# Optimization experiments

Hardware: AMD Instinct MI355X
Metric: run time of the kernel (lower is better)

Reference implementation:

```python
import jax, jax.numpy as jnp
import numpy as np


def _sage_layer(x, src, dst, W_self, W_neigh, b, n_nodes):
    # mean aggregation over incoming edges: agg[v] = mean(x[u] for (u,v) in E)
    agg = jax.ops.segment_sum(x[src], dst, num_segments=n_nodes)          # [N, D]
    cnt = jax.ops.segment_sum(jnp.ones((src.shape[0],), x.dtype), dst,
                              num_segments=n_nodes)                        # [N]
    agg = agg / jnp.clip(cnt, 1.0)[:, None]
    # h = ReLU(x W_self^T + agg W_neigh^T + b)   (torch Linear weight is [out, in])
    h = jnp.einsum('nd,od->no', x, W_self) + jnp.einsum('nd,od->no', agg, W_neigh) + b
    return jax.nn.relu(h)


def setup_inputs() -> dict:
    key = jax.random.key(0)
    ks = jax.random.split(key, 7)
    N, E = 50000, 800000
    F_IN, H, F_OUT = 128, 256, 128
    x = jax.random.normal(ks[0], (N, F_IN), dtype=jnp.float32)
    edge_index = jax.random.randint(ks[1], (2, E), 0, N, dtype=jnp.int64)
    s = 0.05
    return {
        'x': x,
        'edge_index': edge_index,
        'W_self1': jax.random.normal(ks[2], (H, F_IN), dtype=jnp.float32) * s,
        'W_neigh1': jax.random.normal(ks[3], (H, F_IN), dtype=jnp.float32) * s,
        'b1': jnp.zeros((H,), dtype=jnp.float32),
        'W_self2': jax.random.normal(ks[4], (F_OUT, H), dtype=jnp.float32) * s,
        'W_neigh2': jax.random.normal(ks[5], (F_OUT, H), dtype=jnp.float32) * s,
        'b2': jnp.zeros((F_OUT,), dtype=jnp.float32),
    }


def reference(x, edge_index, W_self1, W_neigh1, b1, W_self2, W_neigh2, b2):
    n_nodes = x.shape[0]
    src, dst = edge_index[0], edge_index[1]
    h = _sage_layer(x, src, dst, W_self1, W_neigh1, b1, n_nodes)
    # dropout is identity at inference
    h = _sage_layer(h, src, dst, W_self2, W_neigh2, b2, n_nodes)
    return h
```

## Files before the change

kernel.cpp:

```cpp
#include <hip/hip_runtime.h>


#define CAP 64
#define CPAD 16

typedef __attribute__((ext_vector_type(8))) short bfrag;
typedef __attribute__((ext_vector_type(4))) float ffrag;

__device__ inline unsigned short f2bf(float f) {
    union { float f; unsigned u; } v; v.f = f;
    unsigned r = (v.u + 0x7FFFu + ((v.u >> 16) & 1u)) >> 16;
    return (unsigned short)r;
}

__global__ __launch_bounds__(256) void fill_direct(const int* __restrict__ src,
                                                   const int* __restrict__ dst,
                                                   int* __restrict__ cnt,
                                                   int* __restrict__ adj, int E) {
    int e = blockIdx.x * 256 + threadIdx.x;
    if (e >= E) return;
    int d = dst[e];
    int r = atomicAdd(&cnt[d * CPAD], 1);
    if (r < CAP) adj[d * CAP + r] = src[e];
}

__global__ __launch_bounds__(256) void cast_f32_bf16(const float* __restrict__ in,
                                                     unsigned short* __restrict__ outp,
                                                     long n4) {
    long i = (long)blockIdx.x * 256 + threadIdx.x;
    if (i >= n4) return;
    float4 v = *(const float4*)(in + i * 4);
    ushort4 o;
    o.x = f2bf(v.x); o.y = f2bf(v.y); o.z = f2bf(v.z); o.w = f2bf(v.w);
    *(ushort4*)(outp + i * 4) = o;
}

__global__ __launch_bounds__(256) void cast_weights(
        const float* __restrict__ W0, const float* __restrict__ W1,
        const float* __restrict__ W2, const float* __restrict__ W3,
        unsigned short* __restrict__ O0, unsigned short* __restrict__ O1,
        unsigned short* __restrict__ O2, unsigned short* __restrict__ O3) {
    int i = blockIdx.x * 256 + threadIdx.x;
    int sel = i >> 13, off = i & 8191;
    const float* src = (sel == 0) ? W0 : (sel == 1) ? W1 : (sel == 2) ? W2 : W3;
    unsigned short* dst = (sel == 0) ? O0 : (sel == 1) ? O1 : (sel == 2) ? O2 : O3;
    float4 v = ((const float4*)src)[off];
    ushort4 o;
    o.x = f2bf(v.x); o.y = f2bf(v.y); o.z = f2bf(v.z); o.w = f2bf(v.w);
    ((ushort4*)dst)[off] = o;
}

#define BFLO(u) __uint_as_float((u) << 16)
#define BFHI(u) __uint_as_float((u) & 0xFFFF0000u)

__global__ __launch_bounds__(256) void gather_mean_bf16(
        const unsigned short* __restrict__ Xb, const int* __restrict__ cnt,
        const int* __restrict__ adj, unsigned short* __restrict__ aggb, int N) {
    int gw = (blockIdx.x * 256 + threadIdx.x) >> 6;
    int lane = threadIdx.x & 63;
    if (gw >= N) return;
    int c = cnt[gw * CPAD]; if (c > CAP) c = CAP;
    const int* al = adj + gw * CAP;
    float a0 = 0.f, a1 = 0.f;
    int j = 0;
    for (; j + 3 < c; j += 4) {
        int s0 = al[j], s1 = al[j + 1], s2 = al[j + 2], s3 = al[j + 3];
        unsigned v0 = *(const unsigned*)(Xb + (size_t)s0 * 128 + lane * 2);
        unsigned v1 = *(const unsigned*)(Xb + (size_t)s1 * 128 + lane * 2);
        unsigned v2 = *(const unsigned*)(Xb + (size_t)s2 * 128 + lane * 2);
        unsigned v3 = *(const unsigned*)(Xb + (size_t)s3 * 128 + lane * 2);
        a0 += (BFLO(v0) + BFLO(v1)) + (BFLO(v2) + BFLO(v3));
        a1 += (BFHI(v0) + BFHI(v1)) + (BFHI(v2) + BFHI(v3));
    }
    for (; j < c; ++j) {
        unsigned v0 = *(const unsigned*)(Xb + (size_t)al[j] * 128 + lane * 2);
        a0 += BFLO(v0); a1 += BFHI(v0);
    }
    float scale = (c > 0) ? 1.0f / (float)c : 0.0f;
    unsigned o = (unsigned)f2bf(a0 * scale) | ((unsigned)f2bf(a1 * scale) << 16);
    *(unsigned*)(aggb + (size_t)gw * 128 + lane * 2) = o;
}

__global__ __launch_bounds__(256) void gather_epilogue_bf16(
        const unsigned short* __restrict__ Zb, const float* __restrict__ S2,
        const int* __restrict__ cnt, const int* __restrict__ adj,
        float* __restrict__ out, int N) {
    int gw = (blockIdx.x * 256 + threadIdx.x) >> 6;
    int lane = threadIdx.x & 63;
    if (gw >= N) return;
    int c = cnt[gw * CPAD]; if (c > CAP) c = CAP;
    const int* al = adj + gw * CAP;
    float a0 = 0.f, a1 = 0.f;
    int j = 0;
    for (; j + 3 < c; j += 4) {
        int s0 = al[j], s1 = al[j + 1], s2 = al[j + 2], s3 = al[j + 3];
        unsigned v0 = *(const unsigned*)(Zb + (size_t)s0 * 128 + lane * 2);
        unsigned v1 = *(const unsigned*)(Zb + (size_t)s1 * 128 + lane * 2);
        unsigned v2 = *(const unsigned*)(Zb + (size_t)s2 * 128 + lane * 2);
        unsigned v3 = *(const unsigned*)(Zb + (size_t)s3 * 128 + lane * 2);
        a0 += (BFLO(v0) + BFLO(v1)) + (BFLO(v2) + BFLO(v3));
        a1 += (BFHI(v0) + BFHI(v1)) + (BFHI(v2) + BFHI(v3));
    }
    for (; j < c; ++j) {
        unsigned v0 = *(const unsigned*)(Zb + (size_t)al[j] * 128 + lane * 2);
        a0 += BFLO(v0); a1 += BFHI(v0);
    }
    float scale = (c > 0) ? 1.0f / (float)c : 0.0f;
    float2 sv = *(const float2*)(S2 + (size_t)gw * 128 + lane * 2);
    float2 o;
    o.x = fmaxf(sv.x + a0 * scale, 0.0f);
    o.y = fmaxf(sv.y + a1 * scale, 0.0f);
    *(float2*)(out + (size_t)gw * 128 + lane * 2) = o;
}

#define L1_LOAD(NF, NTV) do {                                                  \
    const short* xr_ = xb   + (size_t)((NTV) * 16 + ln) * 128 + lk * 8;        \
    const short* ar_ = aggb + (size_t)((NTV) * 16 + ln) * 128 + lk * 8;        \
    _Pragma("unroll") for (int kc = 0; kc < 4; ++kc) {                         \
        NF[kc]     = *(const bfrag*)(xr_ + kc * 32);                           \
        NF[4 + kc] = *(const bfrag*)(ar_ + kc * 32); }                         \
} while (0)

#define L1_STEP(NF, CURNT) do {                                                \
    const int node_ = (CURNT) * 16 + ln;                                       \
    ffrag acc_[4];                                                             \
    _Pragma("unroll") for (int m = 0; m < 4; ++m) {                            \
        acc_[m][0] = bv[m].x; acc_[m][1] = bv[m].y;                            \
        acc_[m][2] = bv[m].z; acc_[m][3] = bv[m].w; }                          \
    _Pragma("unroll") for (int m = 0; m < 4; ++m) {                            \
        _Pragma("unroll") for (int kc = 0; kc < 4; ++kc)                       \
            acc_[m] = __builtin_amdgcn_mfma_f32_16x16x32_bf16(                 \
                wfs[m][kc], NF[kc], acc_[m], 0, 0, 0);                         \
        _Pragma("unroll") for (int kc = 0; kc < 4; ++kc)                       \
            acc_[m] = __builtin_amdgcn_mfma_f32_16x16x32_bf16(                 \
                wfn[m][kc], NF[4 + kc], acc_[m], 0, 0, 0); }                   \
    _Pragma("unroll") for (int m = 0; m < 4; ++m) {                            \
        ushort4 o_;                                                            \
        o_.x = f2bf(fmaxf(acc_[m][0], 0.f)); o_.y = f2bf(fmaxf(acc_[m][1], 0.f)); \
        o_.z = f2bf(fmaxf(acc_[m][2], 0.f)); o_.w = f2bf(fmaxf(acc_[m][3], 0.f)); \
        *(ushort4*)(h1b + (size_t)node_ * 256 + (wave * 4 + m) * 16 + lk * 4) = o_; } \
} while (0)

__global__ __launch_bounds__(256) void mfma_layer1(
        const short* __restrict__ xb, const short* __restrict__ aggb,
        const short* __restrict__ Ws, const short* __restrict__ Wn,
        const float* __restrict__ bias, unsigned short* __restrict__ h1b, int NT)
{
    const int wave = threadIdx.x >> 6, lane = threadIdx.x & 63;
    const int ln = lane & 15, lk = lane >> 4;

    bfrag wfs[4][4], wfn[4][4];
    #pragma unroll
    for (int m = 0; m < 4; ++m) {
        const short* ws = Ws + (size_t)((wave * 4 + m) * 16 + ln) * 128 + lk * 8;
        const short* wn = Wn + (size_t)((wave * 4 + m) * 16 + ln) * 128 + lk * 8;
        #pragma unroll
        for (int kc = 0; kc < 4; ++kc) {
            wfs[m][kc] = *(const bfrag*)(ws + kc * 32);
            wfn[m][kc] = *(const bfrag*)(wn + kc * 32);
        }
    }
    float4 bv[4];
    #pragma unroll
    for (int m = 0; m < 4; ++m)
        bv[m] = *(const float4*)(bias + (wave * 4 + m) * 16 + lk * 4);

    bfrag nfA[8], nfB[8];
    const int stride = gridDim.x;
    int nt = blockIdx.x;
    if (nt >= NT) return;
    L1_LOAD(nfA, nt);
    while (true) {
        int ntn = nt + stride;
        if (ntn < NT) L1_LOAD(nfB, ntn);
        L1_STEP(nfA, nt);
        nt = ntn; if (nt >= NT) break;
        ntn = nt + stride;
        if (ntn < NT) L1_LOAD(nfA, ntn);
        L1_STEP(nfB, nt);
        nt = ntn; if (nt >= NT) break;
    }
}

#define L2_LOAD(NF, NTV) do {                                                  \
    const short* hr_ = h1b + (size_t)((NTV) * 16 + ln) * 256 + lk * 8;         \
    _Pragma("unroll") for (int kc = 0; kc < 8; ++kc)                           \
        NF[kc] = *(const bfrag*)(hr_ + kc * 32);                               \
} while (0)

#define L2_STEP(NF, CURNT) do {                                                \
    const int node_ = (CURNT) * 16 + ln;                                       \
    ffrag aS_[2], aZ_[2];                                                      \
    _Pragma("unroll") for (int m = 0; m < 2; ++m) {                            \
        aS_[m][0] = bv[m].x; aS_[m][1] = bv[m].y;                              \
        aS_[m][2] = bv[m].z; aS_[m][3] = bv[m].w;                              \
        aZ_[m][0] = 0.f; aZ_[m][1] = 0.f; aZ_[m][2] = 0.f; aZ_[m][3] = 0.f; }  \
    _Pragma("unroll") for (int m = 0; m < 2; ++m)                              \
        _Pragma("unroll") for (int kc = 0; kc < 8; ++kc) {                     \
            aS_[m] = __builtin_amdgcn_mfma_f32_16x16x32_bf16(                  \
                wfs[m][kc], NF[kc], aS_[m], 0, 0, 0);                          \
            aZ_[m] = __builtin_amdgcn_mfma_f32_16x16x32_bf16(                  \
                wfn[m][kc], NF[kc], aZ_[m], 0, 0, 0); }                        \
    _Pragma("unroll") for (int m = 0; m < 2; ++m) {                            \
        float4 sv_;                                                            \
        sv_.x = aS_[m][0]; sv_.y = aS_[m][1]; sv_.z = aS_[m][2]; sv_.w = aS_[m][3]; \
        *(float4*)(s2 + (size_t)node_ * 128 + (wave * 2 + m) * 16 + lk * 4) = sv_; \
        ushort4 zo_;                                                           \
        zo_.x = f2bf(aZ_[m][0]); zo_.y = f2bf(aZ_[m][1]);                      \
        zo_.z = f2bf(aZ_[m][2]); zo_.w = f2bf(aZ_[m][3]);                      \
        *(ushort4*)(z2b + (size_t)node_ * 128 + (wave * 2 + m) * 16 + lk * 4) = zo_; } \
} while (0)

__global__ __launch_bounds__(256) void mfma_layer2(
        const short* __restrict__ h1b, const short* __restrict__ Ws,
        const short* __restrict__ Wn, const float* __restrict__ bias,
        float* __restrict__ s2, unsigned short* __restrict__ z2b, int NT)
{
    const int wave = threadIdx.x >> 6, lane = threadIdx.x & 63;
    const int ln = lane & 15, lk = lane >> 4;

    bfrag wfs[2][8], wfn[2][8];
    #pragma unroll
    for (int m = 0; m < 2; ++m) {
        const short* ws = Ws + (size_t)((wave * 2 + m) * 16 + ln) * 256 + lk * 8;
        const short* wn = Wn + (size_t)((wave * 2 + m) * 16 + ln) * 256 + lk * 8;
        #pragma unroll
        for (int kc = 0; kc < 8; ++kc) {
            wfs[m][kc] = *(const bfrag*)(ws + kc * 32);
            wfn[m][kc] = *(const bfrag*)(wn + kc * 32);
        }
    }
    float4 bv[2];
    #pragma unroll
    for (int m = 0; m < 2; ++m)
        bv[m] = *(const float4*)(bias + (wave * 2 + m) * 16 + lk * 4);

    bfrag nfA[8], nfB[8];
    const int stride = gridDim.x;
    int nt = blockIdx.x;
    if (nt >= NT) return;
    L2_LOAD(nfA, nt);
    while (true) {
        int ntn = nt + stride;
        if (ntn < NT) L2_LOAD(nfB, ntn);
        L2_STEP(nfA, nt);
        nt = ntn; if (nt >= NT) break;
        ntn = nt + stride;
        if (ntn < NT) L2_LOAD(nfA, ntn);
        L2_STEP(nfB, nt);
        nt = ntn; if (nt >= NT) break;
    }
}

extern "C" void kernel_launch(void* const* d_in, const int* in_sizes, int n_in,
                              void* d_out, int out_size, void* d_ws, size_t ws_size,
                              hipStream_t stream) {
    const float* x   = (const float*)d_in[0];
    const int*   ei  = (const int*)d_in[1];
    const float* Ws1 = (const float*)d_in[2];
    const float* Wn1 = (const float*)d_in[3];
    const float* b1  = (const float*)d_in[4];
    const float* Ws2 = (const float*)d_in[5];
    const float* Wn2 = (const float*)d_in[6];
    const float* b2  = (const float*)d_in[7];
    float* out = (float*)d_out;

    const int N = in_sizes[0] / 128;
    const int E = in_sizes[1] / 2;
    const int NT = N / 16;
    const int* src = ei;
    const int* dst = ei + E;

    unsigned short* xb   = (unsigned short*)d_ws;
    unsigned short* h1b  = xb   + (size_t)N * 128;
    unsigned short* aggb = h1b  + (size_t)N * 256;
    unsigned short* z2b  = aggb + (size_t)N * 128;
    float* s2            = (float*)(z2b + (size_t)N * 128);
    unsigned short* Wsb1 = (unsigned short*)(s2 + (size_t)N * 128);
    unsigned short* Wnb1 = Wsb1 + 32768;
    unsigned short* Wsb2 = Wnb1 + 32768;
    unsigned short* Wnb2 = Wsb2 + 32768;
    int* cnt = (int*)(Wnb2 + 32768);
    int* adj = cnt + (size_t)N * CPAD;

    hipMemsetAsync(cnt, 0, (size_t)N * CPAD * sizeof(int), stream);
    fill_direct<<<(E + 255) / 256, 256, 0, stream>>>(src, dst, cnt, adj, E);

    {
        long n4 = (long)N * 128 / 4;
        cast_f32_bf16<<<(int)((n4 + 255) / 256), 256, 0, stream>>>(x, xb, n4);
        cast_weights<<<128, 256, 0, stream>>>(Ws1, Wn1, Ws2, Wn2,
                                              Wsb1, Wnb1, Wsb2, Wnb2);
    }

    const int gather_blocks = (N * 64 + 255) / 256;

    gather_mean_bf16<<<gather_blocks, 256, 0, stream>>>(xb, cnt, adj, aggb, N);
    mfma_layer1<<<512, 256, 0, stream>>>(
        (const short*)xb, (const short*)aggb, (const short*)Wsb1, (const short*)Wnb1,
        b1, h1b, NT);

    mfma_layer2<<<512, 256, 0, stream>>>(
        (const short*)h1b, (const short*)Wsb2, (const short*)Wnb2, b2, s2, z2b, NT);
    gather_epilogue_bf16<<<gather_blocks, 256, 0, stream>>>(
        z2b, s2, cnt, adj, out, N);
}
```

Before: 263.8 us.

## Fuse prep kernels, shrink adjacency to u16, slice edge fill, batch neighbor loads

Merges the edge fill, feature cast and weight cast into one launch. The fill is split into 8 destination-range slices so that the atomics for nearby nodes tend to run together. The adjacency list is stored as 16-bit indices to halve its traffic. The gathers load 8 indices at once and issue masked loads, giving more memory-level parallelism. The u16 indices only hold while N fits in 65536, and the slicing makes each block reread the dst array 8 times.

```diff
diff --git a/kernel.cpp b/kernel.cpp
--- a/kernel.cpp
+++ b/kernel.cpp
@@ -3,6 +3,7 @@
 
 #define CAP 64
 #define CPAD 16
+#define NSLICE 8
 
 typedef __attribute__((ext_vector_type(8))) short bfrag;
 typedef __attribute__((ext_vector_type(4))) float ffrag;
@@ -13,41 +14,47 @@
     return (unsigned short)r;
 }
 
-__global__ __launch_bounds__(256) void fill_direct(const int* __restrict__ src,
-                                                   const int* __restrict__ dst,
-                                                   int* __restrict__ cnt,
-                                                   int* __restrict__ adj, int E) {
-    int e = blockIdx.x * 256 + threadIdx.x;
-    if (e >= E) return;
-    int d = dst[e];
-    int r = atomicAdd(&cnt[d * CPAD], 1);
-    if (r < CAP) adj[d * CAP + r] = src[e];
-}
-
-__global__ __launch_bounds__(256) void cast_f32_bf16(const float* __restrict__ in,
-                                                     unsigned short* __restrict__ outp,
-                                                     long n4) {
-    long i = (long)blockIdx.x * 256 + threadIdx.x;
-    if (i >= n4) return;
-    float4 v = *(const float4*)(in + i * 4);
-    ushort4 o;
-    o.x = f2bf(v.x); o.y = f2bf(v.y); o.z = f2bf(v.z); o.w = f2bf(v.w);
-    *(ushort4*)(outp + i * 4) = o;
-}
-
-__global__ __launch_bounds__(256) void cast_weights(
+__global__ __launch_bounds__(256) void prep_kernel(
+        const int* __restrict__ src, const int* __restrict__ dst,
+        int* __restrict__ cnt, unsigned short* __restrict__ adj,
+        int E, int nper, int nfill,
+        const float* __restrict__ x, unsigned short* __restrict__ xb, long xn4,
+        int xblocks,
         const float* __restrict__ W0, const float* __restrict__ W1,
         const float* __restrict__ W2, const float* __restrict__ W3,
         unsigned short* __restrict__ O0, unsigned short* __restrict__ O1,
-        unsigned short* __restrict__ O2, unsigned short* __restrict__ O3) {
-    int i = blockIdx.x * 256 + threadIdx.x;
+        unsigned short* __restrict__ O2, unsigned short* __restrict__ O3)
+{
+    int b = blockIdx.x;
+    if (b < nfill) {
+        int slice = b & (NSLICE - 1);
+        int e = (b >> 3) * 256 + (int)threadIdx.x;
+        if (e >= E) return;
+        int d = dst[e];
+        if ((unsigned)(d - slice * nper) >= (unsigned)nper) return;
+        int r = atomicAdd(&cnt[d * CPAD], 1);
+        if (r < CAP) adj[(size_t)d * CAP + r] = (unsigned short)src[e];
+        return;
+    }
+    b -= nfill;
+    if (b < xblocks) {
+        long i = (long)b * 256 + threadIdx.x;
+        if (i >= xn4) return;
+        float4 v = *(const float4*)(x + i * 4);
+        ushort4 o;
+        o.x = f2bf(v.x); o.y = f2bf(v.y); o.z = f2bf(v.z); o.w = f2bf(v.w);
+        *(ushort4*)(xb + i * 4) = o;
+        return;
+    }
+    b -= xblocks;
+    int i = b * 256 + (int)threadIdx.x;
     int sel = i >> 13, off = i & 8191;
-    const float* src = (sel == 0) ? W0 : (sel == 1) ? W1 : (sel == 2) ? W2 : W3;
-    unsigned short* dst = (sel == 0) ? O0 : (sel == 1) ? O1 : (sel == 2) ? O2 : O3;
-    float4 v = ((const float4*)src)[off];
+    const float* srcw = (sel == 0) ? W0 : (sel == 1) ? W1 : (sel == 2) ? W2 : W3;
+    unsigned short* dstw = (sel == 0) ? O0 : (sel == 1) ? O1 : (sel == 2) ? O2 : O3;
+    float4 v = ((const float4*)srcw)[off];
     ushort4 o;
     o.x = f2bf(v.x); o.y = f2bf(v.y); o.z = f2bf(v.z); o.w = f2bf(v.w);
-    ((ushort4*)dst)[off] = o;
+    ((ushort4*)dstw)[off] = o;
 }
 
 #define BFLO(u) __uint_as_float((u) << 16)
@@ -55,26 +62,27 @@
 
 __global__ __launch_bounds__(256) void gather_mean_bf16(
         const unsigned short* __restrict__ Xb, const int* __restrict__ cnt,
-        const int* __restrict__ adj, unsigned short* __restrict__ aggb, int N) {
+        const unsigned short* __restrict__ adj,
+        unsigned short* __restrict__ aggb, int N) {
     int gw = (blockIdx.x * 256 + threadIdx.x) >> 6;
     int lane = threadIdx.x & 63;
     if (gw >= N) return;
     int c = cnt[gw * CPAD]; if (c > CAP) c = CAP;
-    const int* al = adj + gw * CAP;
+    const unsigned short* al = adj + (size_t)gw * CAP;
     float a0 = 0.f, a1 = 0.f;
-    int j = 0;
-    for (; j + 3 < c; j += 4) {
-        int s0 = al[j], s1 = al[j + 1], s2 = al[j + 2], s3 = al[j + 3];
-        unsigned v0 = *(const unsigned*)(Xb + (size_t)s0 * 128 + lane * 2);
-        unsigned v1 = *(const unsigned*)(Xb + (size_t)s1 * 128 + lane * 2);
-        unsigned v2 = *(const unsigned*)(Xb + (size_t)s2 * 128 + lane * 2);
-        unsigned v3 = *(const unsigned*)(Xb + (size_t)s3 * 128 + lane * 2);
-        a0 += (BFLO(v0) + BFLO(v1)) + (BFLO(v2) + BFLO(v3));
-        a1 += (BFHI(v0) + BFHI(v1)) + (BFHI(v2) + BFHI(v3));
-    }
-    for (; j < c; ++j) {
-        unsigned v0 = *(const unsigned*)(Xb + (size_t)al[j] * 128 + lane * 2);
-        a0 += BFLO(v0); a1 += BFHI(v0);
+    int rounds = (c + 7) >> 3;
+    for (int rb = 0; rb < rounds; ++rb) {
+        int j = rb << 3;
+        ushort4 q0 = *(const ushort4*)(al + j);
+        ushort4 q1 = *(const ushort4*)(al + j + 4);
+        unsigned short ss[8] = {q0.x, q0.y, q0.z, q0.w, q1.x, q1.y, q1.z, q1.w};
+        #pragma unroll
+        for (int k = 0; k < 8; ++k) {
+            bool m = (j + k) < c;
+            int s = m ? (int)ss[k] : 0;
+            unsigned v = *(const unsigned*)(Xb + (size_t)s * 128 + lane * 2);
+            if (m) { a0 += BFLO(v); a1 += BFHI(v); }
+        }
     }
     float scale = (c > 0) ? 1.0f / (float)c : 0.0f;
     unsigned o = (unsigned)f2bf(a0 * scale) | ((unsigned)f2bf(a1 * scale) << 16);
@@ -83,27 +91,27 @@
 
 __global__ __launch_bounds__(256) void gather_epilogue_bf16(
         const unsigned short* __restrict__ Zb, const float* __restrict__ S2,
-        const int* __restrict__ cnt, const int* __restrict__ adj,
+        const int* __restrict__ cnt, const unsigned short* __restrict__ adj,
         float* __restrict__ out, int N) {
     int gw = (blockIdx.x * 256 + threadIdx.x) >> 6;
     int lane = threadIdx.x & 63;
     if (gw >= N) return;
     int c = cnt[gw * CPAD]; if (c > CAP) c = CAP;
-    const int* al = adj + gw * CAP;
+    const unsigned short* al = adj + (size_t)gw * CAP;
     float a0 = 0.f, a1 = 0.f;
-    int j = 0;
-    for (; j + 3 < c; j += 4) {
-        int s0 = al[j], s1 = al[j + 1], s2 = al[j + 2], s3 = al[j + 3];
-        unsigned v0 = *(const unsigned*)(Zb + (size_t)s0 * 128 + lane * 2);
-        unsigned v1 = *(const unsigned*)(Zb + (size_t)s1 * 128 + lane * 2);
-        unsigned v2 = *(const unsigned*)(Zb + (size_t)s2 * 128 + lane * 2);
-        unsigned v3 = *(const unsigned*)(Zb + (size_t)s3 * 128 + lane * 2);
-        a0 += (BFLO(v0) + BFLO(v1)) + (BFLO(v2) + BFLO(v3));
-        a1 += (BFHI(v0) + BFHI(v1)) + (BFHI(v2) + BFHI(v3));
-    }
-    for (; j < c; ++j) {
-        unsigned v0 = *(const unsigned*)(Zb + (size_t)al[j] * 128 + lane * 2);
-        a0 += BFLO(v0); a1 += BFHI(v0);
+    int rounds = (c + 7) >> 3;
+    for (int rb = 0; rb < rounds; ++rb) {
+        int j = rb << 3;
+        ushort4 q0 = *(const ushort4*)(al + j);
+        ushort4 q1 = *(const ushort4*)(al + j + 4);
+        unsigned short ss[8] = {q0.x, q0.y, q0.z, q0.w, q1.x, q1.y, q1.z, q1.w};
+        #pragma unroll
+        for (int k = 0; k < 8; ++k) {
+            bool m = (j + k) < c;
+            int s = m ? (int)ss[k] : 0;
+            unsigned v = *(const unsigned*)(Zb + (size_t)s * 128 + lane * 2);
+            if (m) { a0 += BFLO(v); a1 += BFHI(v); }
+        }
     }
     float scale = (c > 0) ? 1.0f / (float)c : 0.0f;
     float2 sv = *(const float2*)(S2 + (size_t)gw * 128 + lane * 2);
@@ -281,17 +289,19 @@
     unsigned short* Wsb2 = Wnb1 + 32768;
     unsigned short* Wnb2 = Wsb2 + 32768;
     int* cnt = (int*)(Wnb2 + 32768);
-    int* adj = cnt + (size_t)N * CPAD;
+    unsigned short* adj = (unsigned short*)(cnt + (size_t)N * CPAD);
+
+    const int nper   = (N + NSLICE - 1) / NSLICE;
+    const int nfill  = ((E + 255) / 256) * NSLICE;
+    const long xn4   = (long)N * 128 / 4;
+    const int xblocks = (int)((xn4 + 255) / 256);
+    const int prep_blocks = nfill + xblocks + 128;
 
     hipMemsetAsync(cnt, 0, (size_t)N * CPAD * sizeof(int), stream);
-    fill_direct<<<(E + 255) / 256, 256, 0, stream>>>(src, dst, cnt, adj, E);
-
-    {
-        long n4 = (long)N * 128 / 4;
-        cast_f32_bf16<<<(int)((n4 + 255) / 256), 256, 0, stream>>>(x, xb, n4);
-        cast_weights<<<128, 256, 0, stream>>>(Ws1, Wn1, Ws2, Wn2,
-                                              Wsb1, Wnb1, Wsb2, Wnb2);
-    }
+    prep_kernel<<<prep_blocks, 256, 0, stream>>>(
+        src, dst, cnt, adj, E, nper, nfill,
+        x, xb, xn4, xblocks,
+        Ws1, Wn1, Ws2, Wn2, Wsb1, Wnb1, Wsb2, Wnb2);
 
     const int gather_blocks = (N * 64 + 255) / 256;
 
```

After: 289.1 us. +9.6%, slower.
